# Optimization experiments

Measured on AMD Instinct MI355X. Metric: run time of the kernel, lower is better.

## Reference

```python
import jax, jax.numpy as jnp
import numpy as np

C = 512
CQK = C // 8  # 64


def setup_inputs() -> dict:
    key = jax.random.key(0)
    ks = jax.random.split(key, 8)
    B, H, W = 16, 32, 32
    x = jax.random.normal(ks[0], (B, C, H, W), dtype=jnp.float32)
    # 1x1 conv weights stored as [out_ch, in_ch] matrices + biases
    sq = 1.0 / np.sqrt(C)
    Wq = jax.random.uniform(ks[1], (CQK, C), jnp.float32, -sq, sq)
    bq = jax.random.uniform(ks[2], (CQK,), jnp.float32, -sq, sq)
    Wk = jax.random.uniform(ks[3], (CQK, C), jnp.float32, -sq, sq)
    bk = jax.random.uniform(ks[4], (CQK,), jnp.float32, -sq, sq)
    Wv = jax.random.uniform(ks[5], (C, C), jnp.float32, -sq, sq)
    bv = jax.random.uniform(ks[6], (C,), jnp.float32, -sq, sq)
    gamma = jax.random.normal(ks[7], (1,), dtype=jnp.float32)
    return {"x": x, "Wq": Wq, "bq": bq, "Wk": Wk, "bk": bk, "Wv": Wv, "bv": bv, "gamma": gamma}


def reference(x, Wq, bq, Wk, bk, Wv, bv, gamma):
    B, Cin, H, W = x.shape
    xf = x.reshape(B, Cin, H * W)  # [B, C, N]
    # 1x1 convs == channel matmuls
    q = jnp.einsum('qc,bcn->bnq', Wq, xf) + bq[None, None, :]   # [B, N, Cqk]
    k = jnp.einsum('qc,bcn->bqn', Wk, xf) + bk[None, :, None]   # [B, Cqk, N]
    v = jnp.einsum('vc,bcn->bvn', Wv, xf) + bv[None, :, None]   # [B, C, N]
    scores = jnp.einsum('bnq,bqm->bnm', q, k)                    # [B, N, N]
    attn = jax.nn.softmax(scores, axis=-1)                       # softmax over keys
    # values @ attn^T : out[b,c,n] = sum_m v[b,c,m] * attn[b,n,m]
    attended = jnp.einsum('bvm,bnm->bvn', v, attn)               # [B, C, N]
    attended = attended.reshape(B, Cin, H, W)
    return gamma[0] * attended + x
```

## Files before the change

kernel.cpp:

```cpp
#include <hip/hip_runtime.h>
#include <stdint.h>

#define BB 16
#define CC 512
#define CQK 64
#define NN 1024

typedef __attribute__((ext_vector_type(8))) short bf16x8;
typedef __attribute__((ext_vector_type(4))) short short4v;
typedef __attribute__((ext_vector_type(8))) unsigned short ushort8;
typedef __attribute__((ext_vector_type(4))) float f32x4;

static __device__ __forceinline__ unsigned short f2bf(float f) {
  uint32_t u = __float_as_uint(f);
  u += 0x7FFFu + ((u >> 16) & 1u);
  return (unsigned short)(u >> 16);
}

static __device__ __forceinline__ void gll16(const unsigned short* g, unsigned short* l) {
  const __attribute__((address_space(1))) unsigned int* gp =
      reinterpret_cast<const __attribute__((address_space(1))) unsigned int*>(
          reinterpret_cast<uintptr_t>(g));
  __attribute__((address_space(3))) unsigned int* lp =
      reinterpret_cast<__attribute__((address_space(3))) unsigned int*>(
          (unsigned int)reinterpret_cast<uintptr_t>(l));
  __builtin_amdgcn_global_load_lds(gp, lp, 16, 0, 0);
}

__global__ __launch_bounds__(256) void k_pack_w(
    const float* __restrict__ Wq, const float* __restrict__ Wk,
    const float* __restrict__ Wv, unsigned short* __restrict__ Wall) {
  int idx = blockIdx.x * 256 + threadIdx.x;
  int e = idx * 4;
  if (e >= 640 * 512) return;
  int o = e >> 9;
  int c = e & 511;
  const float* src;
  if (o < 64)        src = Wq + (size_t)o * 512;
  else if (o < 128)  src = Wk + (size_t)(o - 64) * 512;
  else               src = Wv + (size_t)(o - 128) * 512;
  float4 v = *(const float4*)(src + c);
  short4v pk;
  pk[0] = (short)f2bf(v.x); pk[1] = (short)f2bf(v.y);
  pk[2] = (short)f2bf(v.z); pk[3] = (short)f2bf(v.w);
  *(short4v*)(Wall + e) = pk;
}

__global__ __launch_bounds__(256) void k_transpose_x(
    const float* __restrict__ x, unsigned short* __restrict__ xT) {
  __shared__ float tile[32][33];
  int b = blockIdx.z;
  int c0 = blockIdx.y * 32;
  int n0 = blockIdx.x * 32;
  int t = threadIdx.x;
  int tn = t & 31, tc = t >> 5;
  const float* xp = x + ((size_t)b * CC + c0) * NN + n0;
#pragma unroll
  for (int i = 0; i < 4; i++) {
    int c = tc + i * 8;
    tile[c][tn] = xp[(size_t)c * NN + tn];
  }
  __syncthreads();
  unsigned short* xq = xT + ((size_t)b * NN + n0) * CC + c0;
  int n = t >> 3;
  int cq = (t & 7) * 4;
  short4v pk;
#pragma unroll
  for (int k = 0; k < 4; k++) pk[k] = (short)f2bf(tile[cq + k][n]);
  *(short4v*)(&xq[(size_t)n * CC + cq]) = pk;
}

__global__ __launch_bounds__(256) void k_gemm1(
    const unsigned short* __restrict__ Wall, const unsigned short* __restrict__ xT,
    const float* __restrict__ bq, const float* __restrict__ bk,
    const float* __restrict__ bv,
    unsigned short* __restrict__ qkT, unsigned short* __restrict__ vbuf) {
  __shared__ __align__(16) unsigned short ldsA[128 * 32];
  __shared__ __align__(16) unsigned short ldsB[128 * 32];
  int b = blockIdx.z;
  int o0 = blockIdx.y * 128;
  int n0 = blockIdx.x * 128;
  int t = threadIdx.x;
  int w = t >> 6, l = t & 63;
  int wm = w & 1, wn = w >> 1;
  int lr = l & 15, lq = l >> 4;

  f32x4 acc[4][4];
#pragma unroll
  for (int i = 0; i < 4; i++)
#pragma unroll
    for (int j = 0; j < 4; j++) acc[i][j] = (f32x4){0.f, 0.f, 0.f, 0.f};

  const unsigned short* Ab = Wall + (size_t)o0 * CC;
  const unsigned short* Bb = xT + ((size_t)b * NN + n0) * CC;
  int srow = t >> 2;
  int skq = (t & 3) * 8;
  int ldsw = (t >> 6) * 512;

  for (int kt = 0; kt < CC; kt += 32) {
#pragma unroll
    for (int p = 0; p < 2; p++) {
      int r = p * 64 + srow;
      gll16(&Ab[(size_t)r * CC + kt + skq], &ldsA[p * 2048 + ldsw]);
      gll16(&Bb[(size_t)r * CC + kt + skq], &ldsB[p * 2048 + ldsw]);
    }
    __syncthreads();
    bf16x8 af[4], bfr[4];
#pragma unroll
    for (int i = 0; i < 4; i++)
      af[i] = *(const bf16x8*)(&ldsA[(wm * 64 + i * 16 + lr) * 32 + lq * 8]);
#pragma unroll
    for (int j = 0; j < 4; j++)
      bfr[j] = *(const bf16x8*)(&ldsB[(wn * 64 + j * 16 + lr) * 32 + lq * 8]);
#pragma unroll
    for (int i = 0; i < 4; i++)
#pragma unroll
      for (int j = 0; j < 4; j++)
        acc[i][j] = __builtin_amdgcn_mfma_f32_16x16x32_bf16(af[i], bfr[j], acc[i][j], 0, 0, 0);
    __syncthreads();
  }

  if (o0 == 0) {
#pragma unroll
    for (int i = 0; i < 4; i++) {
      int ob = wm * 64 + i * 16 + lq * 4;
#pragma unroll
      for (int j = 0; j < 4; j++) {
        int n = n0 + wn * 64 + j * 16 + lr;
        short4v pk;
#pragma unroll
        for (int r = 0; r < 4; r++) {
          int o = ob + r;
          float bias = (o < 64) ? bq[o] : bk[o - 64];
          pk[r] = (short)f2bf(acc[i][j][r] + bias);
        }
        *(short4v*)(&qkT[((size_t)b * NN + n) * 128 + ob]) = pk;
      }
    }
  } else {
#pragma unroll
    for (int i = 0; i < 4; i++) {
#pragma unroll
      for (int r = 0; r < 4; r++) {
        int o = o0 + wm * 64 + i * 16 + lq * 4 + r;
        int c = o - 128;
        float bias = bv[c];
#pragma unroll
        for (int j = 0; j < 4; j++) {
          int n = n0 + wn * 64 + j * 16 + lr;
          vbuf[((size_t)b * CC + c) * NN + n] = f2bf(acc[i][j][r] + bias);
        }
      }
    }
  }
}

#define QT 64
#define MC 64
#define PSTR 72

__global__ __launch_bounds__(256, 2) void k_flash(
    const unsigned short* __restrict__ qkT, const unsigned short* __restrict__ vbuf,
    const float* __restrict__ x, const float* __restrict__ gamma,
    float* __restrict__ out) {
  __shared__ __align__(16) unsigned short P[QT * PSTR];
  __shared__ float red[4 * QT];
  __shared__ float fin[QT];

  int b = blockIdx.z;
  int chalf = blockIdx.y;
  int n0 = blockIdx.x * QT;
  int t = threadIdx.x;
  int w = t >> 6, l = t & 63;
  int lr = l & 15, lq = l >> 4;
  const unsigned short* qk = qkT + (size_t)b * NN * 128;
  const unsigned short* Vb = vbuf + ((size_t)b * CC + chalf * 256 + w * 64) * NN;

  bf16x8 aq[4][2];
#pragma unroll
  for (int nj = 0; nj < 4; nj++)
#pragma unroll
    for (int ks = 0; ks < 2; ks++)
      aq[nj][ks] = *(const bf16x8*)(&qk[(size_t)(n0 + nj * 16 + lr) * 128 + ks * 32 + lq * 8]);

  f32x4 acc[4][4];
#pragma unroll
  for (int ci = 0; ci < 4; ci++)
#pragma unroll
    for (int nj = 0; nj < 4; nj++) acc[ci][nj] = (f32x4){0.f, 0.f, 0.f, 0.f};
  float sreg[4][4];
#pragma unroll
  for (int nj = 0; nj < 4; nj++)
#pragma unroll
    for (int r = 0; r < 4; r++) sreg[nj][r] = 0.f;

  float ev[4][4];
  {
    int mrow = w * 16 + lr;
    bf16x8 kf0 = *(const bf16x8*)(&qk[(size_t)mrow * 128 + 64 + lq * 8]);
    bf16x8 kf1 = *(const bf16x8*)(&qk[(size_t)mrow * 128 + 96 + lq * 8]);
#pragma unroll
    for (int nj = 0; nj < 4; nj++) {
      f32x4 s = (f32x4){0.f, 0.f, 0.f, 0.f};
      s = __builtin_amdgcn_mfma_f32_16x16x32_bf16(aq[nj][0], kf0, s, 0, 0, 0);
      s = __builtin_amdgcn_mfma_f32_16x16x32_bf16(aq[nj][1], kf1, s, 0, 0, 0);
#pragma unroll
      for (int r = 0; r < 4; r++) {
        float e = __expf(s[r]);
        ev[nj][r] = e;
        sreg[nj][r] += e;
      }
    }
  }

  for (int m0 = 0; m0 < NN; m0 += MC) {
    bf16x8 af0[4];
#pragma unroll
    for (int ci = 0; ci < 4; ci++)
      af0[ci] = *(const bf16x8*)(&Vb[(size_t)(ci * 16 + lr) * NN + m0 + lq * 8]);

    __syncthreads();
#pragma unroll
    for (int nj = 0; nj < 4; nj++)
#pragma unroll
      for (int r = 0; r < 4; r++)
        P[(nj * 16 + lq * 4 + r) * PSTR + w * 16 + lr] = f2bf(ev[nj][r]);

    if (m0 + MC < NN) {
      int mrow = m0 + MC + w * 16 + lr;
      bf16x8 kf0 = *(const bf16x8*)(&qk[(size_t)mrow * 128 + 64 + lq * 8]);
      bf16x8 kf1 = *(const bf16x8*)(&qk[(size_t)mrow * 128 + 96 + lq * 8]);
#pragma unroll
      for (int nj = 0; nj < 4; nj++) {
        f32x4 s = (f32x4){0.f, 0.f, 0.f, 0.f};
        s = __builtin_amdgcn_mfma_f32_16x16x32_bf16(aq[nj][0], kf0, s, 0, 0, 0);
        s = __builtin_amdgcn_mfma_f32_16x16x32_bf16(aq[nj][1], kf1, s, 0, 0, 0);
#pragma unroll
        for (int r = 0; r < 4; r++) {
          float e = __expf(s[r]);
          ev[nj][r] = e;
          sreg[nj][r] += e;
        }
      }
    }
    __syncthreads();

    bf16x8 af1[4];
#pragma unroll
    for (int ci = 0; ci < 4; ci++)
      af1[ci] = *(const bf16x8*)(&Vb[(size_t)(ci * 16 + lr) * NN + m0 + 32 + lq * 8]);

#pragma unroll
    for (int nj = 0; nj < 4; nj++) {
      bf16x8 pf = *(const bf16x8*)(&P[(nj * 16 + lr) * PSTR + lq * 8]);
#pragma unroll
      for (int ci = 0; ci < 4; ci++)
        acc[ci][nj] = __builtin_amdgcn_mfma_f32_16x16x32_bf16(af0[ci], pf, acc[ci][nj], 0, 0, 0);
    }
#pragma unroll
    for (int nj = 0; nj < 4; nj++) {
      bf16x8 pf = *(const bf16x8*)(&P[(nj * 16 + lr) * PSTR + 32 + lq * 8]);
#pragma unroll
      for (int ci = 0; ci < 4; ci++)
        acc[ci][nj] = __builtin_amdgcn_mfma_f32_16x16x32_bf16(af1[ci], pf, acc[ci][nj], 0, 0, 0);
    }
  }

#pragma unroll
  for (int nj = 0; nj < 4; nj++)
#pragma unroll
    for (int r = 0; r < 4; r++) {
#pragma unroll
      for (int d = 1; d < 16; d <<= 1) sreg[nj][r] += __shfl_xor(sreg[nj][r], d, 64);
    }
  __syncthreads();
  if (lr == 0) {
#pragma unroll
    for (int nj = 0; nj < 4; nj++)
#pragma unroll
      for (int r = 0; r < 4; r++) red[w * QT + nj * 16 + lq * 4 + r] = sreg[nj][r];
  }
  __syncthreads();
  if (t < QT) {
    float ssum = red[t] + red[QT + t] + red[2 * QT + t] + red[3 * QT + t];
    fin[t] = ssum;
  }
  __syncthreads();

  float invL[4];
#pragma unroll
  for (int nj = 0; nj < 4; nj++) invL[nj] = 1.0f / fin[nj * 16 + lr];
  float g = gamma[0];
#pragma unroll
  for (int ci = 0; ci < 4; ci++) {
#pragma unroll
    for (int r = 0; r < 4; r++) {
      int c = chalf * 256 + w * 64 + ci * 16 + lq * 4 + r;
#pragma unroll
      for (int nj = 0; nj < 4; nj++) {
        size_t idx = ((size_t)b * CC + c) * NN + n0 + nj * 16 + lr;
        out[idx] = g * acc[ci][nj][r] * invL[nj] + x[idx];
      }
    }
  }
}

extern "C" void kernel_launch(void* const* d_in, const int* in_sizes, int n_in,
                              void* d_out, int out_size, void* d_ws, size_t ws_size,
                              hipStream_t stream) {
  (void)in_sizes; (void)n_in; (void)out_size; (void)ws_size;
  const float* x     = (const float*)d_in[0];
  const float* Wq    = (const float*)d_in[1];
  const float* bq    = (const float*)d_in[2];
  const float* Wk    = (const float*)d_in[3];
  const float* bk    = (const float*)d_in[4];
  const float* Wv    = (const float*)d_in[5];
  const float* bv    = (const float*)d_in[6];
  const float* gamma = (const float*)d_in[7];
  float* out = (float*)d_out;

  char* ws = (char*)d_ws;
  unsigned short* Wall = (unsigned short*)(ws);
  unsigned short* xT   = (unsigned short*)(ws + 655360);
  unsigned short* qkT  = (unsigned short*)(ws + 655360 + 16777216);
  unsigned short* vbuf = (unsigned short*)(ws + 655360 + 16777216 + 4194304);

  k_pack_w<<<dim3(320), dim3(256), 0, stream>>>(Wq, Wk, Wv, Wall);
  k_transpose_x<<<dim3(NN / 32, CC / 32, BB), dim3(256), 0, stream>>>(x, xT);
  k_gemm1<<<dim3(NN / 128, 640 / 128, BB), dim3(256), 0, stream>>>(Wall, xT, bq, bk, bv, qkT, vbuf);
  k_flash<<<dim3(NN / QT, 2, BB), dim3(256), 0, stream>>>(qkT, vbuf, x, gamma, out);
}
```

Before: 171.3 us.

## Double-buffer GEMM LDS tiles, swizzle block order for XCDs, prefetch K fragments

The projection GEMM now double-buffers its LDS tiles so the global-to-LDS loads for the next k-step are issued before the MFMAs on the current one, overlapping memory latency with compute. Both GEMM and attention kernels switch to a 1D grid with a block-index swizzle across 8 groups, intended to keep blocks that share data on the same XCD/L2. The attention kernel hoists the next K-fragment global loads ahead of the barrier so their latency overlaps the P-tile write. This doubles GEMM LDS use and adds registers for the prefetched fragments.

```diff
diff --git a/kernel.cpp b/kernel.cpp
--- a/kernel.cpp
+++ b/kernel.cpp
@@ -75,11 +75,16 @@
     const float* __restrict__ bq, const float* __restrict__ bk,
     const float* __restrict__ bv,
     unsigned short* __restrict__ qkT, unsigned short* __restrict__ vbuf) {
-  __shared__ __align__(16) unsigned short ldsA[128 * 32];
-  __shared__ __align__(16) unsigned short ldsB[128 * 32];
-  int b = blockIdx.z;
-  int o0 = blockIdx.y * 128;
-  int n0 = blockIdx.x * 128;
+  __shared__ __align__(16) unsigned short ldsA[2][128 * 32];
+  __shared__ __align__(16) unsigned short ldsB[2][128 * 32];
+  int bid = blockIdx.x;
+  int swz = (bid & 7) * 80 + (bid >> 3);
+  int nx = swz & 7;
+  int rest = swz >> 3;
+  int oy = rest % 5;
+  int b = rest / 5;
+  int o0 = oy * 128;
+  int n0 = nx * 128;
   int t = threadIdx.x;
   int w = t >> 6, l = t & 63;
   int wm = w & 1, wn = w >> 1;
@@ -97,21 +102,32 @@
   int skq = (t & 3) * 8;
   int ldsw = (t >> 6) * 512;
 
-  for (int kt = 0; kt < CC; kt += 32) {
-#pragma unroll
-    for (int p = 0; p < 2; p++) {
-      int r = p * 64 + srow;
-      gll16(&Ab[(size_t)r * CC + kt + skq], &ldsA[p * 2048 + ldsw]);
-      gll16(&Bb[(size_t)r * CC + kt + skq], &ldsB[p * 2048 + ldsw]);
-    }
-    __syncthreads();
+#pragma unroll
+  for (int p = 0; p < 2; p++) {
+    int r = p * 64 + srow;
+    gll16(&Ab[(size_t)r * CC + skq], &ldsA[0][p * 2048 + ldsw]);
+    gll16(&Bb[(size_t)r * CC + skq], &ldsB[0][p * 2048 + ldsw]);
+  }
+  __syncthreads();
+
+  for (int s = 0; s < 16; ++s) {
+    int cur = s & 1;
+    if (s + 1 < 16) {
+      int kt = (s + 1) * 32;
+#pragma unroll
+      for (int p = 0; p < 2; p++) {
+        int r = p * 64 + srow;
+        gll16(&Ab[(size_t)r * CC + kt + skq], &ldsA[cur ^ 1][p * 2048 + ldsw]);
+        gll16(&Bb[(size_t)r * CC + kt + skq], &ldsB[cur ^ 1][p * 2048 + ldsw]);
+      }
+    }
     bf16x8 af[4], bfr[4];
 #pragma unroll
     for (int i = 0; i < 4; i++)
-      af[i] = *(const bf16x8*)(&ldsA[(wm * 64 + i * 16 + lr) * 32 + lq * 8]);
+      af[i] = *(const bf16x8*)(&ldsA[cur][(wm * 64 + i * 16 + lr) * 32 + lq * 8]);
 #pragma unroll
     for (int j = 0; j < 4; j++)
-      bfr[j] = *(const bf16x8*)(&ldsB[(wn * 64 + j * 16 + lr) * 32 + lq * 8]);
+      bfr[j] = *(const bf16x8*)(&ldsB[cur][(wn * 64 + j * 16 + lr) * 32 + lq * 8]);
 #pragma unroll
     for (int i = 0; i < 4; i++)
 #pragma unroll
@@ -167,9 +183,12 @@
   __shared__ float red[4 * QT];
   __shared__ float fin[QT];
 
-  int b = blockIdx.z;
-  int chalf = blockIdx.y;
-  int n0 = blockIdx.x * QT;
+  int bid = blockIdx.x;
+  int swz = (bid & 7) * 64 + (bid >> 3);
+  int ntile = swz & 15;
+  int chalf = (swz >> 4) & 1;
+  int b = swz >> 5;
+  int n0 = ntile * QT;
   int t = threadIdx.x;
   int w = t >> 6, l = t & 63;
   int lr = l & 15, lq = l >> 4;
@@ -219,6 +238,13 @@
     for (int ci = 0; ci < 4; ci++)
       af0[ci] = *(const bf16x8*)(&Vb[(size_t)(ci * 16 + lr) * NN + m0 + lq * 8]);
 
+    bf16x8 kf0n, kf1n;
+    if (m0 + MC < NN) {
+      int mrow = m0 + MC + w * 16 + lr;
+      kf0n = *(const bf16x8*)(&qk[(size_t)mrow * 128 + 64 + lq * 8]);
+      kf1n = *(const bf16x8*)(&qk[(size_t)mrow * 128 + 96 + lq * 8]);
+    }
+
     __syncthreads();
 #pragma unroll
     for (int nj = 0; nj < 4; nj++)
@@ -227,14 +253,11 @@
         P[(nj * 16 + lq * 4 + r) * PSTR + w * 16 + lr] = f2bf(ev[nj][r]);
 
     if (m0 + MC < NN) {
-      int mrow = m0 + MC + w * 16 + lr;
-      bf16x8 kf0 = *(const bf16x8*)(&qk[(size_t)mrow * 128 + 64 + lq * 8]);
-      bf16x8 kf1 = *(const bf16x8*)(&qk[(size_t)mrow * 128 + 96 + lq * 8]);
 #pragma unroll
       for (int nj = 0; nj < 4; nj++) {
         f32x4 s = (f32x4){0.f, 0.f, 0.f, 0.f};
-        s = __builtin_amdgcn_mfma_f32_16x16x32_bf16(aq[nj][0], kf0, s, 0, 0, 0);
-        s = __builtin_amdgcn_mfma_f32_16x16x32_bf16(aq[nj][1], kf1, s, 0, 0, 0);
+        s = __builtin_amdgcn_mfma_f32_16x16x32_bf16(aq[nj][0], kf0n, s, 0, 0, 0);
+        s = __builtin_amdgcn_mfma_f32_16x16x32_bf16(aq[nj][1], kf1n, s, 0, 0, 0);
 #pragma unroll
         for (int r = 0; r < 4; r++) {
           float e = __expf(s[r]);
@@ -327,6 +350,6 @@
 
   k_pack_w<<<dim3(320), dim3(256), 0, stream>>>(Wq, Wk, Wv, Wall);
   k_transpose_x<<<dim3(NN / 32, CC / 32, BB), dim3(256), 0, stream>>>(x, xT);
-  k_gemm1<<<dim3(NN / 128, 640 / 128, BB), dim3(256), 0, stream>>>(Wall, xT, bq, bk, bv, qkT, vbuf);
-  k_flash<<<dim3(NN / QT, 2, BB), dim3(256), 0, stream>>>(qkT, vbuf, x, gamma, out);
-}
+  k_gemm1<<<dim3(640), dim3(256), 0, stream>>>(Wall, xT, bq, bk, bv, qkT, vbuf);
+  k_flash<<<dim3(512), dim3(256), 0, stream>>>(qkT, vbuf, x, gamma, out);
+}
```

New measurement: 166.6 us. 1.03x faster.
